# Kernel tuning notes

Measured on AMD Instinct MI355X. Metric: run time of the kernel, lower is better.

The kernel has to match this reference:

```python
import jax, jax.numpy as jnp
import numpy as np

B, T, C = 4, 2048, 1024
NH = 16
HD = C // NH


def setup_inputs() -> dict:
    key = jax.random.key(0)
    k1, k2, k3 = jax.random.split(key, 3)
    x = jax.random.normal(k1, (B, T, C), dtype=jnp.float32)
    Wqkv = jax.random.normal(k2, (C, 3 * C), dtype=jnp.float32) * 0.02
    bqkv = jnp.zeros((3 * C,), dtype=jnp.float32)
    Wproj = jax.random.normal(k3, (C, C), dtype=jnp.float32) * 0.02
    bproj = jnp.zeros((C,), dtype=jnp.float32)
    return {"x": x, "Wqkv": Wqkv, "bqkv": bqkv, "Wproj": Wproj, "bproj": bproj}


def reference(x, Wqkv, bqkv, Wproj, bproj):
    Bx, Tx, Cx = x.shape
    qkv = x @ Wqkv + bqkv  # [B,T,3C]
    q, k, v = jnp.split(qkv, 3, axis=-1)
    # [B, NH, T, HD]
    q = q.reshape(Bx, Tx, NH, HD).transpose(0, 2, 1, 3)
    k = k.reshape(Bx, Tx, NH, HD).transpose(0, 2, 1, 3)
    v = v.reshape(Bx, Tx, NH, HD).transpose(0, 2, 1, 3)
    scale = 1.0 / jnp.sqrt(jnp.float32(HD))
    att = jnp.einsum('bhqd,bhkd->bhqk', q, k) * scale  # [B,NH,T,T]
    causal = jnp.tril(jnp.ones((Tx, Tx), dtype=bool))
    att = jnp.where(causal, att, jnp.float32(-jnp.inf))
    att = jax.nn.softmax(att, axis=-1)
    y = jnp.einsum('bhqk,bhkd->bhqd', att, v)  # [B,NH,T,HD]
    y = y.transpose(0, 2, 1, 3).reshape(Bx, Tx, Cx)
    return y @ Wproj + bproj
```

## Files before the change

kernel.cpp:

```cpp
#include <hip/hip_runtime.h>
#include <hip/hip_bf16.h>
#include <math.h>

#define B_  4
#define T_  2048
#define C_  1024
#define NH_ 16
#define HD_ 64

using bf16 = __hip_bfloat16;
typedef __attribute__((ext_vector_type(8))) short bf16x8;
typedef __attribute__((ext_vector_type(4))) short bf16x4;
typedef __attribute__((ext_vector_type(4))) float f32x4;

__device__ __forceinline__ bf16 f2b(float f){ return __float2bfloat16(f); }

__device__ __forceinline__ short f2bs(float f){
  union { float f; unsigned u; } x; x.f = f;
  x.u += 0x7FFFu + ((x.u >> 16) & 1u);
  return (short)(x.u >> 16);
}

__device__ __forceinline__ bf16x4 pack_bf16x4(float a, float b, float c, float d){
  union { bf16x4 v; __hip_bfloat162 h[2]; } u;
  u.h[0] = __float22bfloat162_rn(make_float2(a, b));
  u.h[1] = __float22bfloat162_rn(make_float2(c, d));
  return u.v;
}

__device__ __forceinline__ void async_load16(const bf16* g, bf16* l){
  __builtin_amdgcn_global_load_lds((const __attribute__((address_space(1))) unsigned int*)g,
                                   (__attribute__((address_space(3))) unsigned int*)l,
                                   16, 0, 0);
}

#define QSCALE 0.18033688011112042f


__global__ __launch_bounds__(256) void k_cvt4(const float* __restrict__ in, bf16* __restrict__ out, int n){
  int i = (blockIdx.x * 256 + threadIdx.x) * 4;
  if (i < n){
    float4 f = *(const float4*)(in + i);
    ushort4 u;
    u.x = (unsigned short)f2bs(f.x);
    u.y = (unsigned short)f2bs(f.y);
    u.z = (unsigned short)f2bs(f.z);
    u.w = (unsigned short)f2bs(f.w);
    *(ushort4*)(out + i) = u;
  }
}

__global__ __launch_bounds__(256) void k_cvtT2(const float* __restrict__ in0, bf16* __restrict__ out0,
                                               const float* __restrict__ in1, bf16* __restrict__ out1){
  __shared__ float t[32][33];
  int b = blockIdx.x;
  const float* in; bf16* out; int Cc, bx, by;
  if (b < 3072){ in = in0; out = out0; Cc = 3*C_; bx = (b % 96)*32; by = (b / 96)*32; }
  else { b -= 3072; in = in1; out = out1; Cc = C_; bx = (b & 31)*32; by = (b >> 5)*32; }
  const int R = C_;
  int lx = threadIdx.x & 31, ly = threadIdx.x >> 5;
  #pragma unroll
  for (int s = 0; s < 4; s++){
    int k = by + ly + s*8;
    t[ly + s*8][lx] = in[(size_t)k * Cc + bx + lx];
  }
  __syncthreads();
  #pragma unroll
  for (int s = 0; s < 4; s++){
    int n = bx + ly + s*8;
    out[(size_t)n * R + by + lx] = f2b(t[lx][ly + s*8]);
  }
}

template<int MODE, int BM>
__global__ __launch_bounds__(BM*2) void k_gemm(
    const bf16* __restrict__ A, const bf16* __restrict__ BT,
    const float* __restrict__ bias,
    bf16* __restrict__ qo, bf16* __restrict__ ko, bf16* __restrict__ vo,
    float* __restrict__ fout,
    int M, int N, int K)
{
  constexpr int NTHR = BM*2;
  constexpr int WMW  = BM/64;
  constexpr int NB   = 512/NTHR;
  __shared__ bf16 As[2][BM*32];
  __shared__ bf16 Bs[2][128*32];

  const int tid  = threadIdx.x;
  const int wave = tid >> 6, lane = tid & 63;
  const int wm = wave % WMW, wn = wave / WMW;
  const int quad = lane >> 4, l15 = lane & 15;
  const int bm = blockIdx.x * BM;
  const int bn = blockIdx.y * 128;

  const bf16* gA[2]; bf16* lA[2];
  #pragma unroll
  for (int s = 0; s < 2; s++){
    const int c = tid + s*NTHR;
    const int r = c >> 2, p = (c & 3) ^ ((r >> 1) & 3);
    gA[s] = A + (size_t)(bm + r)*K + p*8;
    lA[s] = &As[0][0] + (size_t)c*8;
  }
  const bf16* gB[NB]; bf16* lB[NB];
  #pragma unroll
  for (int s = 0; s < NB; s++){
    const int c = tid + s*NTHR;
    const int r = c >> 2, p = (c & 3) ^ ((r >> 1) & 3);
    gB[s] = BT + (size_t)(bn + r)*K + p*8;
    lB[s] = &Bs[0][0] + (size_t)c*8;
  }
  const int fsw = (l15 >> 1) & 3;

  f32x4 acc[4][4] = {};
  const int nK = K >> 5;

  #pragma unroll
  for (int s = 0; s < 2; s++) async_load16(gA[s], lA[s]);
  #pragma unroll
  for (int s = 0; s < NB; s++) async_load16(gB[s], lB[s]);

  for (int kt = 0; kt < nK; kt++){
    __syncthreads();
    if (kt + 1 < nK){
      const int off = (kt + 1) * 32;
      const int ba  = ((kt + 1) & 1) * (BM*32);
      const int bb  = ((kt + 1) & 1) * 4096;
      #pragma unroll
      for (int s = 0; s < 2; s++) async_load16(gA[s] + off, lA[s] + ba);
      #pragma unroll
      for (int s = 0; s < NB; s++) async_load16(gB[s] + off, lB[s] + bb);
    }
    const bf16* as = &As[kt & 1][0];
    const bf16* bs = &Bs[kt & 1][0];

    bf16x8 af[4], bfv[4];
    #pragma unroll
    for (int i = 0; i < 4; i++)
      af[i]  = *reinterpret_cast<const bf16x8*>(as + (wm*64 + i*16 + l15)*32 + ((quad ^ fsw) << 3));
    #pragma unroll
    for (int j = 0; j < 4; j++)
      bfv[j] = *reinterpret_cast<const bf16x8*>(bs + (wn*64 + j*16 + l15)*32 + ((quad ^ fsw) << 3));
    #pragma unroll
    for (int i = 0; i < 4; i++)
      #pragma unroll
      for (int j = 0; j < 4; j++)
        acc[i][j] = __builtin_amdgcn_mfma_f32_16x16x32_bf16(af[i], bfv[j], acc[i][j], 0, 0, 0);
  }

  if (MODE == 0){
    const int sec = bn >> 10;
    const int bb2 = bm >> 11;
    const int tb  = (bm & (T_ - 1)) + wm*64 + quad*4;
    const int hn  = ((bn & 1023) >> 6) + wn;
    const size_t bhx = (size_t)(bb2 * NH_ + hn);
    if (sec == 2){
      #pragma unroll
      for (int j = 0; j < 4; j++){
        const int d = j*16 + l15;
        const float bj = bias[bn + wn*64 + j*16 + l15];
        bf16* vrow = vo + (bhx * HD_ + d) * (size_t)T_;
        const int sw = (l15 & 7) * 8;
        #pragma unroll
        for (int i = 0; i < 4; i++){
          const int t = (tb + i*16) ^ sw;
          *reinterpret_cast<bf16x4*>(vrow + t) =
            pack_bf16x4(acc[i][j][0] + bj, acc[i][j][1] + bj,
                        acc[i][j][2] + bj, acc[i][j][3] + bj);
        }
      }
    } else {
      bf16* dst = (sec == 0) ? qo : ko;
      const float sc = (sec == 0) ? QSCALE : 1.0f;
      #pragma unroll
      for (int j = 0; j < 4; j++){
        const int d = j*16 + l15;
        const float bj = bias[bn + wn*64 + j*16 + l15];
        bf16* base = dst + bhx * T_ * HD_;
        #pragma unroll
        for (int i = 0; i < 4; i++){
          const int t0 = tb + i*16;
          #pragma unroll
          for (int r = 0; r < 4; r++){
            const int dq = d ^ (((quad*4 + r) & 7) * 8);
            short s = f2bs((acc[i][j][r] + bj) * sc);
            base[(size_t)(t0 + r) * HD_ + dq] = *(bf16*)&s;
          }
        }
      }
    }
  } else {
    #pragma unroll
    for (int i = 0; i < 4; i++){
      #pragma unroll
      for (int j = 0; j < 4; j++){
        const int n = bn + wn*64 + j*16 + l15;
        const float bj = bias[n];
        float* p0 = fout + (size_t)(bm + wm*64 + i*16 + quad*4) * N + n;
        #pragma unroll
        for (int r = 0; r < 4; r++)
          p0[(size_t)r * N] = acc[i][j][r] + bj;
      }
    }
  }
}

__global__ __launch_bounds__(256) void k_attn(
    const bf16* __restrict__ Q, const bf16* __restrict__ Kg,
    const bf16* __restrict__ Vt, bf16* __restrict__ Y)
{
  __shared__ bf16 Ks[2][64*64];
  __shared__ bf16 Vs[2][64*64];

  const int bh = blockIdx.x;
  const int bb = bh >> 4, hh = bh & 15;
  const int qt = 15 - blockIdx.y;
  const int tid  = threadIdx.x;
  const int wave = tid >> 6, lane = tid & 63;
  const int quad = lane >> 4, l15 = lane & 15;
  const int swz  = (l15 & 7) * 8;

  const size_t baseQK = (size_t)bh * T_ * HD_;
  const size_t baseV  = (size_t)bh * HD_ * T_;

  const int ca = wave, cb = wave + 4;
  const bf16* kg_a = Kg + baseQK + ca*512 + (size_t)lane*8;
  const bf16* kg_b = Kg + baseQK + cb*512 + (size_t)lane*8;
  const bf16* vg_a = Vt + baseV + (size_t)(ca*8 + (lane>>3)) * T_ + (lane&7)*8;
  const bf16* vg_b = Vt + baseV + (size_t)(cb*8 + (lane>>3)) * T_ + (lane&7)*8;
  bf16* kl_a0 = &Ks[0][0] + ca*512;  bf16* kl_b0 = &Ks[0][0] + cb*512;
  bf16* vl_a0 = &Vs[0][0] + ca*512;  bf16* vl_b0 = &Vs[0][0] + cb*512;

  bf16x4 ones_f;
  {
    short v = (l15 == 0) ? f2bs(1.0f) : (short)0;
    ones_f = (bf16x4){ v, v, v, v };
  }

  const int jmax = 2*qt + 1;

  bf16x8 qf[2][2];
  #pragma unroll
  for (int s = 0; s < 2; s++){
    const int t = qt*128 + s*64 + wave*16 + l15;
    #pragma unroll
    for (int ks = 0; ks < 2; ks++){
      const int col = (ks*32 + quad*8) ^ swz;
      qf[s][ks] = *reinterpret_cast<const bf16x8*>(Q + baseQK + (size_t)t*HD_ + col);
    }
  }

  async_load16(kg_a, kl_a0);  async_load16(kg_b, kl_b0);
  async_load16(vg_a, vl_a0);  async_load16(vg_b, vl_b0);

  f32x4 o[2][5] = {};

  for (int j = 0; j <= jmax; j++){
    __syncthreads();

    if (j < jmax){
      const int nb = ((j+1) & 1) * 4096;
      const size_t ko = (size_t)(j+1) * 64 * HD_;
      async_load16(kg_a + ko, kl_a0 + nb);  async_load16(kg_b + ko, kl_b0 + nb);
      async_load16(vg_a + (j+1)*64, vl_a0 + nb);
      async_load16(vg_b + (j+1)*64, vl_b0 + nb);
    }

    const bf16* ksb = &Ks[j & 1][0];
    const bf16* vsb = &Vs[j & 1][0];

    f32x4 st[2][4] = {};
    __builtin_amdgcn_s_setprio(1);
    #pragma unroll
    for (int ks = 0; ks < 2; ks++){
      #pragma unroll
      for (int tk = 0; tk < 4; tk++){
        bf16x8 kf = *reinterpret_cast<const bf16x8*>(ksb + (tk*16 + l15)*64 + ((ks*32 + quad*8) ^ swz));
        st[0][tk] = __builtin_amdgcn_mfma_f32_16x16x32_bf16(kf, qf[0][ks], st[0][tk], 0, 0, 0);
        st[1][tk] = __builtin_amdgcn_mfma_f32_16x16x32_bf16(kf, qf[1][ks], st[1][tk], 0, 0, 0);
      }
    }
    __builtin_amdgcn_s_setprio(0);

    bf16x4 pf[2][4];
    #pragma unroll
    for (int s = 0; s < 2; s++){
      const int qg = qt*128 + s*64 + wave*16 + l15;
      const bool msk = s ? (j > 2*qt) : (j >= 2*qt);
      #pragma unroll
      for (int tk = 0; tk < 4; tk++){
        float e[4];
        #pragma unroll
        for (int r = 0; r < 4; r++){
          float sv = st[s][tk][r];
          if (msk){
            const int kvg = j*64 + tk*16 + quad*4 + r;
            if (kvg > qg) sv = -1e30f;
          }
          e[r] = exp2f(sv);
        }
        pf[s][tk] = pack_bf16x4(e[0], e[1], e[2], e[3]);
      }
    }

    __builtin_amdgcn_s_setprio(1);
    #pragma unroll
    for (int td = 0; td < 4; td++){
      #pragma unroll
      for (int tk = 0; tk < 4; tk++){
        bf16x4 vf = *reinterpret_cast<const bf16x4*>(vsb + (td*16 + l15)*64 + ((tk*16 + quad*4) ^ swz));
        o[0][td] = __builtin_amdgcn_mfma_f32_16x16x16bf16_1k(vf, pf[0][tk], o[0][td], 0, 0, 0);
        o[1][td] = __builtin_amdgcn_mfma_f32_16x16x16bf16_1k(vf, pf[1][tk], o[1][td], 0, 0, 0);
      }
    }
    #pragma unroll
    for (int tk = 0; tk < 4; tk++){
      o[0][4] = __builtin_amdgcn_mfma_f32_16x16x16bf16_1k(ones_f, pf[0][tk], o[0][4], 0, 0, 0);
      o[1][4] = __builtin_amdgcn_mfma_f32_16x16x16bf16_1k(ones_f, pf[1][tk], o[1][4], 0, 0, 0);
    }
    __builtin_amdgcn_s_setprio(0);
  }

  #pragma unroll
  for (int s = 0; s < 2; s++){
    const float l = __shfl(o[s][4][0], l15, 64);
    const float inv = 1.0f / l;
    const int t = qt*128 + s*64 + wave*16 + l15;
    bf16* yrow = Y + ((size_t)(bb * T_ + t)) * C_ + hh * HD_;
    #pragma unroll
    for (int td = 0; td < 4; td++){
      *reinterpret_cast<bf16x4*>(yrow + td*16 + quad*4) =
        pack_bf16x4(o[s][td][0] * inv, o[s][td][1] * inv,
                    o[s][td][2] * inv, o[s][td][3] * inv);
    }
  }
}


extern "C" void kernel_launch(void* const* d_in, const int* in_sizes, int n_in,
                              void* d_out, int out_size, void* d_ws, size_t ws_size,
                              hipStream_t stream) {
  const float* x     = (const float*)d_in[0];
  const float* Wqkv  = (const float*)d_in[1];
  const float* bqkv  = (const float*)d_in[2];
  const float* Wproj = (const float*)d_in[3];
  const float* bproj = (const float*)d_in[4];
  float* out = (float*)d_out;

  const size_t M = (size_t)B_ * T_;
  char* w = (char*)d_ws;
  bf16* xb     = (bf16*)w;  w += M * C_ * 2;
  bf16* WqkvT  = (bf16*)w;  w += (size_t)3 * C_ * C_ * 2;
  bf16* WprojT = (bf16*)w;  w += (size_t)C_ * C_ * 2;
  bf16* Qb     = (bf16*)w;  w += M * C_ * 2;
  bf16* Kb     = (bf16*)w;  w += M * C_ * 2;
  bf16* Vtb    = (bf16*)w;  w += M * C_ * 2;
  bf16* Yb     = (bf16*)w;  w += M * C_ * 2;

  {
    int n = (int)(M * C_);
    k_cvt4<<<dim3((n/4 + 255)/256), dim3(256), 0, stream>>>(x, xb, n);
  }
  k_cvtT2<<<dim3(4096), dim3(256), 0, stream>>>(Wqkv, WqkvT, Wproj, WprojT);
  k_gemm<0,256><<<dim3(M/256, (3*C_)/128), dim3(512), 0, stream>>>(
      xb, WqkvT, bqkv, Qb, Kb, Vtb, nullptr, (int)M, 3*C_, C_);
  k_attn<<<dim3(64, 16), dim3(256), 0, stream>>>(Qb, Kb, Vtb, Yb);
  k_gemm<1,128><<<dim3(M/128, C_/128), dim3(256), 0, stream>>>(
      Yb, WprojT, bproj, nullptr, nullptr, nullptr, out, (int)M, C_, C_);
}
```

Measured before the change: 258.5 us.

## Triple-buffer GEMM LDS pipeline with vmcnt waits and merge prep kernels

Moves the GEMM main loop from double to triple buffering. Loads are issued two k-tiles ahead, and an explicit s_waitcnt vmcnt is paired with a raw s_barrier in place of __syncthreads, so more global-to-LDS traffic stays in flight. It also merges the x conversion kernel and the weight transpose kernel into one launch to save a kernel launch. The cost is more LDS per block, which may lower occupancy, and the hand-counted vmcnt values could be wrong if the number of outstanding loads per thread differs from what is assumed.

Measured after the change: 265.2 us. 2.6% more time.

```diff
diff --git a/kernel.cpp b/kernel.cpp
--- a/kernel.cpp
+++ b/kernel.cpp
@@ -36,24 +36,25 @@
 
 #define QSCALE 0.18033688011112042f
 
-
-__global__ __launch_bounds__(256) void k_cvt4(const float* __restrict__ in, bf16* __restrict__ out, int n){
-  int i = (blockIdx.x * 256 + threadIdx.x) * 4;
-  if (i < n){
-    float4 f = *(const float4*)(in + i);
-    ushort4 u;
-    u.x = (unsigned short)f2bs(f.x);
-    u.y = (unsigned short)f2bs(f.y);
-    u.z = (unsigned short)f2bs(f.z);
-    u.w = (unsigned short)f2bs(f.w);
-    *(ushort4*)(out + i) = u;
-  }
-}
-
-__global__ __launch_bounds__(256) void k_cvtT2(const float* __restrict__ in0, bf16* __restrict__ out0,
-                                               const float* __restrict__ in1, bf16* __restrict__ out1){
+__global__ __launch_bounds__(256) void k_prep(const float* __restrict__ x, bf16* __restrict__ xb, int n,
+                                              const float* __restrict__ in0, bf16* __restrict__ out0,
+                                              const float* __restrict__ in1, bf16* __restrict__ out1){
   __shared__ float t[32][33];
   int b = blockIdx.x;
+  if (b < 8192){
+    int i = (b * 256 + threadIdx.x) * 4;
+    if (i < n){
+      float4 f = *(const float4*)(x + i);
+      ushort4 u;
+      u.x = (unsigned short)f2bs(f.x);
+      u.y = (unsigned short)f2bs(f.y);
+      u.z = (unsigned short)f2bs(f.z);
+      u.w = (unsigned short)f2bs(f.w);
+      *(ushort4*)(xb + i) = u;
+    }
+    return;
+  }
+  b -= 8192;
   const float* in; bf16* out; int Cc, bx, by;
   if (b < 3072){ in = in0; out = out0; Cc = 3*C_; bx = (b % 96)*32; by = (b / 96)*32; }
   else { b -= 3072; in = in1; out = out1; Cc = C_; bx = (b & 31)*32; by = (b >> 5)*32; }
@@ -67,8 +68,8 @@
   __syncthreads();
   #pragma unroll
   for (int s = 0; s < 4; s++){
-    int n = bx + ly + s*8;
-    out[(size_t)n * R + by + lx] = f2b(t[lx][ly + s*8]);
+    int n2 = bx + ly + s*8;
+    out[(size_t)n2 * R + by + lx] = f2b(t[lx][ly + s*8]);
   }
 }
 
@@ -83,8 +84,8 @@
   constexpr int NTHR = BM*2;
   constexpr int WMW  = BM/64;
   constexpr int NB   = 512/NTHR;
-  __shared__ bf16 As[2][BM*32];
-  __shared__ bf16 Bs[2][128*32];
+  __shared__ bf16 As[3][BM*32];
+  __shared__ bf16 Bs[3][128*32];
 
   const int tid  = threadIdx.x;
   const int wave = tid >> 6, lane = tid & 63;
@@ -118,20 +119,33 @@
   for (int s = 0; s < 2; s++) async_load16(gA[s], lA[s]);
   #pragma unroll
   for (int s = 0; s < NB; s++) async_load16(gB[s], lB[s]);
+  #pragma unroll
+  for (int s = 0; s < 2; s++) async_load16(gA[s] + 32, lA[s] + BM*32);
+  #pragma unroll
+  for (int s = 0; s < NB; s++) async_load16(gB[s] + 32, lB[s] + 128*32);
 
   for (int kt = 0; kt < nK; kt++){
-    __syncthreads();
     if (kt + 1 < nK){
-      const int off = (kt + 1) * 32;
-      const int ba  = ((kt + 1) & 1) * (BM*32);
-      const int bb  = ((kt + 1) & 1) * 4096;
+      if constexpr (NB == 1) asm volatile("s_waitcnt vmcnt(3)" ::: "memory");
+      else                   asm volatile("s_waitcnt vmcnt(4)" ::: "memory");
+    } else {
+      asm volatile("s_waitcnt vmcnt(0)" ::: "memory");
+    }
+    __builtin_amdgcn_s_barrier();
+    __builtin_amdgcn_sched_barrier(0);
+
+    if (kt + 2 < nK){
+      const int off = (kt + 2) * 32;
+      const int bi  = (kt + 2) % 3;
+      const int ba  = bi * (BM*32);
+      const int bb  = bi * 4096;
       #pragma unroll
       for (int s = 0; s < 2; s++) async_load16(gA[s] + off, lA[s] + ba);
       #pragma unroll
       for (int s = 0; s < NB; s++) async_load16(gB[s] + off, lB[s] + bb);
     }
-    const bf16* as = &As[kt & 1][0];
-    const bf16* bs = &Bs[kt & 1][0];
+    const bf16* as = &As[kt % 3][0];
+    const bf16* bs = &Bs[kt % 3][0];
 
     bf16x8 af[4], bfv[4];
     #pragma unroll
@@ -358,9 +372,8 @@
 
   {
     int n = (int)(M * C_);
-    k_cvt4<<<dim3((n/4 + 255)/256), dim3(256), 0, stream>>>(x, xb, n);
-  }
-  k_cvtT2<<<dim3(4096), dim3(256), 0, stream>>>(Wqkv, WqkvT, Wproj, WprojT);
+    k_prep<<<dim3(12288), dim3(256), 0, stream>>>(x, xb, n, Wqkv, WqkvT, Wproj, WprojT);
+  }
   k_gemm<0,256><<<dim3(M/256, (3*C_)/128), dim3(512), 0, stream>>>(
       xb, WqkvT, bqkv, Qb, Kb, Vtb, nullptr, (int)M, 3*C_, C_);
   k_attn<<<dim3(64, 16), dim3(256), 0, stream>>>(Qb, Kb, Vtb, Yb);
```
